# Optimization experiments

Measured on AMD Instinct MI355X. Metric: run time of the kernel, lower is better.

The kernel has to match this reference:

```python
import jax, jax.numpy as jnp
import numpy as np

N_NODES = 100000


def _sage_conv(x, src, dst, Wl, Wr, b):
    # PyG SAGEConv (aggr='mean'): out = lin_l(mean_j x_j) + lin_r(x_i)
    deg = jax.ops.segment_sum(jnp.ones_like(src, dtype=x.dtype), dst, num_segments=N_NODES)
    agg = jax.ops.segment_sum(x[src], dst, num_segments=N_NODES)
    agg = agg / jnp.clip(deg, 1.0)[:, None]
    return agg @ Wl.T + x @ Wr.T + b


def setup_inputs() -> dict:
    key = jax.random.key(0)
    ks = jax.random.split(key, 16)
    N, E, ES = N_NODES, 1600000, 100000
    IN, H, D = 64, 128, 64

    def lin(k, out_c, in_c):
        s = 1.0 / np.sqrt(in_c)
        return jax.random.uniform(k, (out_c, in_c), jnp.float32, -s, s)

    inp = {
        "x": jax.random.normal(ks[0], (N, IN), jnp.float32),
        "edge_index": jax.random.randint(ks[1], (2, E), 0, N, jnp.int64),
        "edge_sample": jax.random.randint(ks[2], (2, ES), 0, N, jnp.int64),
        # SAGEConv 0: 64 -> 128
        "Wl0": lin(ks[3], H, IN), "Wr0": lin(ks[4], H, IN), "b0": jnp.zeros((H,), jnp.float32),
        # SAGEConv 1: 128 -> 128
        "Wl1": lin(ks[5], H, H), "Wr1": lin(ks[6], H, H), "b1": jnp.zeros((H,), jnp.float32),
        # SAGEConv 2: 128 -> 64
        "Wl2": lin(ks[7], D, H), "Wr2": lin(ks[8], D, H), "b2": jnp.zeros((D,), jnp.float32),
        # feature decoder MLP: 64 -> 128 -> 64
        "Wd1": lin(ks[9], H, D), "bd1": jnp.zeros((H,), jnp.float32),
        "Wd2": lin(ks[10], IN, H), "bd2": jnp.zeros((IN,), jnp.float32),
    }
    return inp


def reference(x, edge_index, edge_sample, Wl0, Wr0, b0, Wl1, Wr1, b1, Wl2, Wr2, b2, Wd1, bd1, Wd2, bd2):
    src, dst = edge_index[0], edge_index[1]
    # encoder (dropout = identity at inference)
    h = jax.nn.relu(_sage_conv(x, src, dst, Wl0, Wr0, b0))
    h = jax.nn.relu(_sage_conv(h, src, dst, Wl1, Wr1, b1))
    emb = _sage_conv(h, src, dst, Wl2, Wr2, b2)
    # feature decoder
    rec = jax.nn.relu(emb @ Wd1.T + bd1) @ Wd2.T + bd2
    # edge decoder: dot product
    edge_scores = jnp.sum(emb[edge_sample[0]] * emb[edge_sample[1]], axis=1)
    return emb, rec, edge_scores
```

## Files before the change

### kernel.cpp

```cpp
#include <hip/hip_runtime.h>

#define NN 100000
#define NBK 98
#define CHUNK 8192
typedef unsigned int uint;
typedef unsigned short ushort;

using f32x4 = __attribute__((ext_vector_type(4))) float;
using s16x8 = __attribute__((ext_vector_type(8))) short;

__device__ inline ushort f32_to_bf16(float f) {
  uint u = __float_as_uint(f);
  uint r = (u + 0x7FFFu + ((u >> 16) & 1u)) >> 16;
  return (ushort)r;
}
__device__ inline float bf16_to_f32(ushort h) {
  return __uint_as_float(((uint)h) << 16);
}

typedef __attribute__((address_space(1))) const unsigned int gas_u32;
typedef __attribute__((address_space(3))) unsigned int las_u32;
__device__ __forceinline__ void gld_lds16(const void* gp, void* lp) {
  __builtin_amdgcn_global_load_lds((gas_u32*)gp, (las_u32*)lp, 16, 0, 0);
}

struct P8 { const float* p[8]; };

__global__ void k_prep(const int* __restrict__ dst, uint* __restrict__ bcnt,
                       uint* __restrict__ chunkCnt, int E, int NCB,
                       const float* __restrict__ x, ushort* __restrict__ xb, int n4, int NC,
                       P8 w, ushort* __restrict__ whi, int wtotal) {
  int b = blockIdx.x;
  int tid = threadIdx.x;
  if (b < NCB) {
    __shared__ uint hist[NBK];
    for (int i = tid; i < NBK; i += 256) hist[i] = 0;
    __syncthreads();
    int base = b * CHUNK;
    int lim = min(base + CHUNK, E);
    for (int e = base + tid; e < lim; e += 256) atomicAdd(&hist[(uint)dst[e] >> 10], 1u);
    __syncthreads();
    for (int i = tid; i < NBK; i += 256) {
      uint h = hist[i];
      chunkCnt[(i << 8) + b] = h;
      if (h) atomicAdd(&bcnt[i], h);
    }
  } else if (b < NCB + NC) {
    int i = (b - NCB) * 256 + tid;
    if (i < n4) {
      float4 v = ((const float4*)x)[i];
      uint2 o;
      o.x = (uint)f32_to_bf16(v.x) | ((uint)f32_to_bf16(v.y) << 16);
      o.y = (uint)f32_to_bf16(v.z) | ((uint)f32_to_bf16(v.w) << 16);
      ((uint2*)xb)[i] = o;
    }
  } else {
    int g = (b - NCB - NC) * 256 + tid;
    if (g < wtotal) {
      const int offs[8] = {0, 8192, 16384, 32768, 49152, 57344, 65536, 73728};
      int s = 0;
#pragma unroll
      for (int i = 1; i < 8; ++i) s += (g >= offs[i]);
      whi[g] = f32_to_bf16(w.p[s][g - offs[s]]);
    }
  }
}

__global__ void k_bscan0(const uint* __restrict__ bcnt, uint* __restrict__ bbase,
                         int* __restrict__ rp) {
  if (threadIdx.x == 0) {
    uint s = 0;
    for (int i = 0; i < NBK; ++i) {
      bbase[i] = s;
      s += bcnt[i];
    }
    bbase[NBK] = s;
    rp[NN] = (int)s;
  }
}

__global__ void k_bscan1(const uint* __restrict__ bbase, const uint* __restrict__ chunkCnt,
                         uint* __restrict__ chunkBase, int NCB) {
  int bk = blockIdx.x;
  int l = threadIdx.x;
  uint carry = bbase[bk];
#pragma unroll
  for (int seg = 0; seg < 4; ++seg) {
    int c = seg * 64 + l;
    uint v = (c < NCB) ? chunkCnt[(bk << 8) + c] : 0u;
    uint incl = v;
#pragma unroll
    for (int off = 1; off < 64; off <<= 1) {
      uint t = __shfl_up(incl, off, 64);
      if (l >= off) incl += t;
    }
    if (c < NCB) chunkBase[(bk << 8) + c] = carry + incl - v;
    carry += __shfl(incl, 63, 64);
  }
}

__global__ void k_bscatter(const int* __restrict__ src, const int* __restrict__ dst,
                           const uint* __restrict__ chunkBase, uint* __restrict__ packed, int E) {
  __shared__ uint cur[NBK];
  int tid = threadIdx.x;
  int b = blockIdx.x;
  for (int i = tid; i < NBK; i += 256) cur[i] = chunkBase[(i << 8) + b];
  __syncthreads();
  int base = b * CHUNK;
  int lim = min(base + CHUNK, E);
  for (int e = base + tid; e < lim; e += 256) {
    uint d = (uint)dst[e];
    uint s = (uint)src[e];
    uint bk = d >> 10;
    uint p = atomicAdd(&cur[bk], 1u);
    packed[p] = ((d & 1023u) << 20) | s;
  }
}

__global__ void k_build(const uint* __restrict__ bbase, const uint* __restrict__ packed,
                        int* __restrict__ rp, int* __restrict__ col) {
  __shared__ uint hist[1024];
  __shared__ uint ws[256];
  int b = blockIdx.x;
  int tid = threadIdx.x;
  uint lo = bbase[b], hi = bbase[b + 1];
#pragma unroll
  for (int i = 0; i < 4; ++i) hist[tid + i * 256] = 0;
  __syncthreads();
  for (uint e = lo + tid; e < hi; e += 256) atomicAdd(&hist[packed[e] >> 20], 1u);
  __syncthreads();
  uint v0 = hist[tid * 4], v1 = hist[tid * 4 + 1], v2 = hist[tid * 4 + 2], v3 = hist[tid * 4 + 3];
  ws[tid] = v0 + v1 + v2 + v3;
  __syncthreads();
  for (int off = 1; off < 256; off <<= 1) {
    uint add = (tid >= off) ? ws[tid - off] : 0u;
    __syncthreads();
    ws[tid] += add;
    __syncthreads();
  }
  uint ex = (tid > 0) ? ws[tid - 1] : 0u;
  hist[tid * 4] = ex;
  hist[tid * 4 + 1] = ex + v0;
  hist[tid * 4 + 2] = ex + v0 + v1;
  hist[tid * 4 + 3] = ex + v0 + v1 + v2;
  int nodeBase = b << 10;
#pragma unroll
  for (int i = 0; i < 4; ++i) {
    int node = nodeBase + tid * 4 + i;
    if (node < NN) rp[node] = (int)(lo + hist[tid * 4 + i]);
  }
  __syncthreads();
  for (uint e = lo + tid; e < hi; e += 256) {
    uint pk = packed[e];
    uint p = atomicAdd(&hist[pk >> 20], 1u);
    col[lo + p] = (int)(pk & 0xFFFFFu);
  }
}

#define ACC1(vv) { alo += __uint_as_float((vv) << 16); ahi += __uint_as_float((vv) & 0xffff0000u); }

template <int F, int MODE>
__global__ void k_agg(const ushort* __restrict__ x, const int* __restrict__ rp,
                      const int* __restrict__ col, const float* __restrict__ u,
                      float* __restrict__ of, ushort* __restrict__ ob, int n) {
  constexpr int RS = F / 2;
  int wave = (blockIdx.x * blockDim.x + threadIdx.x) >> 6;
  int lane = threadIdx.x & 63;
  int node, l;
  if (F == 128) { node = wave; l = lane; }
  else { node = wave * 2 + (lane >> 5); l = lane & 31; }
  if (node >= n) return;
  int beg = rp[node], end = rp[node + 1];
  int deg = end - beg;
  const uint* __restrict__ xu = (const uint*)x;
  float alo = 0.f, ahi = 0.f;
  int j = beg;
  for (; j + 8 <= end; j += 8) {
    int c0 = col[j], c1 = col[j + 1], c2 = col[j + 2], c3 = col[j + 3];
    int c4 = col[j + 4], c5 = col[j + 5], c6 = col[j + 6], c7 = col[j + 7];
    uint v0 = xu[(size_t)c0 * RS + l];
    uint v1 = xu[(size_t)c1 * RS + l];
    uint v2 = xu[(size_t)c2 * RS + l];
    uint v3 = xu[(size_t)c3 * RS + l];
    uint v4 = xu[(size_t)c4 * RS + l];
    uint v5 = xu[(size_t)c5 * RS + l];
    uint v6 = xu[(size_t)c6 * RS + l];
    uint v7 = xu[(size_t)c7 * RS + l];
    ACC1(v0) ACC1(v1) ACC1(v2) ACC1(v3) ACC1(v4) ACC1(v5) ACC1(v6) ACC1(v7)
  }
  if (j + 4 <= end) {
    int c0 = col[j], c1 = col[j + 1], c2 = col[j + 2], c3 = col[j + 3];
    uint v0 = xu[(size_t)c0 * RS + l];
    uint v1 = xu[(size_t)c1 * RS + l];
    uint v2 = xu[(size_t)c2 * RS + l];
    uint v3 = xu[(size_t)c3 * RS + l];
    ACC1(v0) ACC1(v1) ACC1(v2) ACC1(v3)
    j += 4;
  }
  for (; j < end; ++j) {
    uint v0 = xu[(size_t)col[j] * RS + l];
    ACC1(v0)
  }
  float inv = 1.0f / (float)(deg > 0 ? deg : 1);
  alo *= inv;
  ahi *= inv;
  if (MODE == 0) {
    ((uint*)ob)[(size_t)node * RS + l] = (uint)f32_to_bf16(alo) | ((uint)f32_to_bf16(ahi) << 16);
  } else {
    float2 uv = ((const float2*)u)[(size_t)node * RS + l];
    float e0 = alo + uv.x, e1 = ahi + uv.y;
    ((float2*)of)[(size_t)node * RS + l] = make_float2(e0, e1);
    ((uint*)ob)[(size_t)node * RS + l] = (uint)f32_to_bf16(e0) | ((uint)f32_to_bf16(e1) << 16);
  }
}

template <int K, int H, bool RELU, bool DUAL, int OUTM>
__global__ __launch_bounds__(256) void k_gemm(
    const ushort* __restrict__ A, const ushort* __restrict__ Wa,
    const ushort* __restrict__ B, const ushort* __restrict__ Wb,
    const float* __restrict__ bias,
    float* __restrict__ outf, ushort* __restrict__ outb, int n) {
  constexpr int BM = 128;
  constexpr int KT = 64;
  constexpr int NKT = K / KT;
  constexpr int MF = (H == 128) ? 4 : 2;
  constexpr int WCH = H / 32;
  __shared__ ushort As[BM * KT];
  __shared__ ushort Ws[H * KT];

  const int tid = threadIdx.x;
  const int lane = tid & 63;
  const int wid = tid >> 6;
  const int fr = lane & 15;
  const int fq = lane >> 4;
  const int blockRow = blockIdx.x * BM;
  const int rowBase = (H == 128) ? (wid >> 1) * 64 : wid * 32;
  const int colBase = (H == 128) ? (wid & 1) * 64 : 0;
  const int srow = lane >> 3;
  const int sslot = (lane & 7) ^ srow;
  const bool fullTile = (blockRow + BM <= n);

  f32x4 acc[MF][4];
#pragma unroll
  for (int mi = 0; mi < MF; ++mi)
#pragma unroll
    for (int ni = 0; ni < 4; ++ni) acc[mi][ni] = (f32x4){0.f, 0.f, 0.f, 0.f};

#pragma unroll
  for (int phase = 0; phase < (DUAL ? 2 : 1); ++phase) {
    const ushort* __restrict__ Ap = phase ? B : A;
    const ushort* __restrict__ Wp = phase ? Wb : Wa;
#pragma unroll
    for (int kt = 0; kt < NKT; ++kt) {
      const int ktb = kt * KT;
      __syncthreads();
      if (fullTile) {
#pragma unroll
        for (int i = 0; i < 4; ++i) {
          int r0 = (wid + i * 4) * 8;
          gld_lds16(Ap + (size_t)(blockRow + r0 + srow) * K + ktb + sslot * 8,
                    (char*)As + r0 * 128);
        }
#pragma unroll
        for (int i = 0; i < WCH; ++i) {
          int r0 = (wid + i * 4) * 8;
          if (WCH >= 4 || wid + i * 4 < WCH * 4)
            gld_lds16(Wp + (size_t)(r0 + srow) * K + ktb + sslot * 8,
                      (char*)Ws + r0 * 128);
        }
      } else {
        for (int c = tid; c < BM * 8; c += 256) {
          int r = c >> 3, kc = c & 7;
          int row = blockRow + r;
          uint4 v = make_uint4(0u, 0u, 0u, 0u);
          if (row < n) v = *(const uint4*)(Ap + (size_t)row * K + ktb + kc * 8);
          *(uint4*)((char*)As + r * 128 + ((kc * 16) ^ ((r & 7) << 4))) = v;
        }
        for (int c = tid; c < H * 8; c += 256) {
          int r = c >> 3, kc = c & 7;
          *(uint4*)((char*)Ws + r * 128 + ((kc * 16) ^ ((r & 7) << 4))) =
              *(const uint4*)(Wp + (size_t)r * K + ktb + kc * 8);
        }
      }
      __syncthreads();
#pragma unroll
      for (int ks = 0; ks < 2; ++ks) {
        const int kb = ks * 64 + fq * 16;
        s16x8 af[MF], wf[4];
#pragma unroll
        for (int mi = 0; mi < MF; ++mi) {
          int r = rowBase + mi * 16 + fr;
          af[mi] = *(const s16x8*)((const char*)As + r * 128 + (kb ^ ((r & 7) << 4)));
        }
#pragma unroll
        for (int ni = 0; ni < 4; ++ni) {
          int r = colBase + ni * 16 + fr;
          wf[ni] = *(const s16x8*)((const char*)Ws + r * 128 + (kb ^ ((r & 7) << 4)));
        }
#pragma unroll
        for (int mi = 0; mi < MF; ++mi)
#pragma unroll
          for (int ni = 0; ni < 4; ++ni)
            acc[mi][ni] = __builtin_amdgcn_mfma_f32_16x16x32_bf16(af[mi], wf[ni], acc[mi][ni], 0, 0, 0);
      }
    }
  }
#pragma unroll
  for (int mi = 0; mi < MF; ++mi) {
#pragma unroll
    for (int ni = 0; ni < 4; ++ni) {
#pragma unroll
      for (int r = 0; r < 4; ++r) {
        int row = blockRow + rowBase + mi * 16 + fq * 4 + r;
        int colI = colBase + ni * 16 + fr;
        if (row < n) {
          float v = acc[mi][ni][r];
          if (OUTM == 3) {
            if (colI < 64)
              outb[(size_t)row * 64 + colI] = f32_to_bf16(v);
            else
              outf[(size_t)row * 64 + (colI - 64)] = v + bias[colI - 64];
          } else {
            if (bias) v += bias[colI];
            if (RELU) v = fmaxf(v, 0.f);
            if (OUTM == 1) outf[(size_t)row * H + colI] = v;
            else outb[(size_t)row * H + colI] = f32_to_bf16(v);
          }
        }
      }
    }
  }
}

__global__ __launch_bounds__(256) void k_dec(
    const ushort* __restrict__ emb, const ushort* __restrict__ Wd1,
    const float* __restrict__ bd1, const ushort* __restrict__ Wd2,
    const float* __restrict__ bd2, float* __restrict__ rec, int n) {
  __shared__ ushort smem[24 * 1024];
  ushort* As = smem;
  ushort* W1 = smem + 8192;
  ushort* W2 = smem + 16384;
  ushort* Hs = smem;

  const int tid = threadIdx.x;
  const int lane = tid & 63;
  const int wid = tid >> 6;
  const int fr = lane & 15;
  const int fq = lane >> 4;
  const int blockRow = blockIdx.x * 128;
  const int rowBase1 = (wid >> 1) * 64;
  const int colBase1 = (wid & 1) * 64;
  const int srow8 = lane >> 3, sl8 = lane & 7;
  const int srow4 = lane >> 4, sl16 = lane & 15;
  const bool fullTile = (blockRow + 128 <= n);

  if (fullTile) {
#pragma unroll
    for (int i = 0; i < 4; ++i) {
      int r0 = (wid + i * 4) * 8;
      gld_lds16(emb + (size_t)(blockRow + r0 + srow8) * 64 + (sl8 ^ srow8) * 8,
                (char*)As + r0 * 128);
    }
#pragma unroll
    for (int i = 0; i < 4; ++i) {
      int r0 = (wid + i * 4) * 8;
      gld_lds16(Wd1 + (size_t)(r0 + srow8) * 64 + (sl8 ^ srow8) * 8, (char*)W1 + r0 * 128);
    }
#pragma unroll
    for (int i = 0; i < 4; ++i) {
      int r0 = (wid + i * 4) * 4;
      int grow = r0 + srow4;
      gld_lds16(Wd2 + (size_t)grow * 128 + (sl16 ^ (grow & 7)) * 8, (char*)W2 + r0 * 256);
    }
  } else {
    for (int c = tid; c < 128 * 8; c += 256) {
      int r = c >> 3, s = c & 7;
      int row = blockRow + r;
      uint4 v = make_uint4(0u, 0u, 0u, 0u);
      if (row < n) v = *(const uint4*)(emb + (size_t)row * 64 + s * 8);
      *(uint4*)((char*)As + r * 128 + ((s ^ (r & 7)) << 4)) = v;
    }
    for (int c = tid; c < 128 * 8; c += 256) {
      int r = c >> 3, s = c & 7;
      *(uint4*)((char*)W1 + r * 128 + ((s ^ (r & 7)) << 4)) =
          *(const uint4*)(Wd1 + (size_t)r * 64 + s * 8);
    }
    for (int c = tid; c < 64 * 16; c += 256) {
      int r = c >> 4, s = c & 15;
      *(uint4*)((char*)W2 + r * 256 + ((s ^ (r & 7)) << 4)) =
          *(const uint4*)(Wd2 + (size_t)r * 128 + s * 8);
    }
  }
  __syncthreads();

  f32x4 a1[4][4];
#pragma unroll
  for (int mi = 0; mi < 4; ++mi)
#pragma unroll
    for (int ni = 0; ni < 4; ++ni) a1[mi][ni] = (f32x4){0.f, 0.f, 0.f, 0.f};
#pragma unroll
  for (int ks = 0; ks < 2; ++ks) {
    s16x8 af[4], wf[4];
#pragma unroll
    for (int mi = 0; mi < 4; ++mi) {
      int r = rowBase1 + mi * 16 + fr;
      af[mi] = *(const s16x8*)((const char*)As + r * 128 + (((ks * 4 + fq) ^ (r & 7)) << 4));
    }
#pragma unroll
    for (int ni = 0; ni < 4; ++ni) {
      int r = colBase1 + ni * 16 + fr;
      wf[ni] = *(const s16x8*)((const char*)W1 + r * 128 + (((ks * 4 + fq) ^ (r & 7)) << 4));
    }
#pragma unroll
    for (int mi = 0; mi < 4; ++mi)
#pragma unroll
      for (int ni = 0; ni < 4; ++ni)
        a1[mi][ni] = __builtin_amdgcn_mfma_f32_16x16x32_bf16(af[mi], wf[ni], a1[mi][ni], 0, 0, 0);
  }
  __syncthreads();
#pragma unroll
  for (int mi = 0; mi < 4; ++mi) {
#pragma unroll
    for (int ni = 0; ni < 4; ++ni) {
#pragma unroll
      for (int r = 0; r < 4; ++r) {
        int rowl = rowBase1 + mi * 16 + fq * 4 + r;
        int colI = colBase1 + ni * 16 + fr;
        float v = fmaxf(a1[mi][ni][r] + bd1[colI], 0.f);
        int byte = rowl * 256 + ((((colI >> 3) ^ (rowl & 7))) << 4) + (colI & 7) * 2;
        *(ushort*)((char*)Hs + byte) = f32_to_bf16(v);
      }
    }
  }
  __syncthreads();

  f32x4 a2[2][4];
#pragma unroll
  for (int mi = 0; mi < 2; ++mi)
#pragma unroll
    for (int ni = 0; ni < 4; ++ni) a2[mi][ni] = (f32x4){0.f, 0.f, 0.f, 0.f};
#pragma unroll
  for (int kk = 0; kk < 4; ++kk) {
    s16x8 af[2], wf[4];
#pragma unroll
    for (int mi = 0; mi < 2; ++mi) {
      int r = wid * 32 + mi * 16 + fr;
      af[mi] = *(const s16x8*)((const char*)Hs + r * 256 + (((kk * 4 + fq) ^ (r & 7)) << 4));
    }
#pragma unroll
    for (int ni = 0; ni < 4; ++ni) {
      int r = ni * 16 + fr;
      wf[ni] = *(const s16x8*)((const char*)W2 + r * 256 + (((kk * 4 + fq) ^ (r & 7)) << 4));
    }
#pragma unroll
    for (int mi = 0; mi < 2; ++mi)
#pragma unroll
      for (int ni = 0; ni < 4; ++ni)
        a2[mi][ni] = __builtin_amdgcn_mfma_f32_16x16x32_bf16(af[mi], wf[ni], a2[mi][ni], 0, 0, 0);
  }
#pragma unroll
  for (int mi = 0; mi < 2; ++mi) {
#pragma unroll
    for (int ni = 0; ni < 4; ++ni) {
#pragma unroll
      for (int r = 0; r < 4; ++r) {
        int row = blockRow + wid * 32 + mi * 16 + fq * 4 + r;
        int colI = ni * 16 + fr;
        if (row < n) rec[(size_t)row * 64 + colI] = a2[mi][ni][r] + bd2[colI];
      }
    }
  }
}

__global__ void k_dot(const float* __restrict__ emb, const int* __restrict__ ea,
                      const int* __restrict__ eb, float* __restrict__ out, int ne) {
  int hw = (blockIdx.x * blockDim.x + threadIdx.x) >> 5;
  int l = threadIdx.x & 31;
  if (hw >= ne) return;
  float2 a = ((const float2*)(emb + (size_t)ea[hw] * 64))[l];
  float2 b = ((const float2*)(emb + (size_t)eb[hw] * 64))[l];
  float v = a.x * b.x + a.y * b.y;
#pragma unroll
  for (int off = 16; off; off >>= 1) v += __shfl_xor(v, off, 64);
  if (l == 0) out[hw] = v;
}

extern "C" void kernel_launch(void* const* d_in, const int* in_sizes, int n_in,
                              void* d_out, int out_size, void* d_ws, size_t ws_size,
                              hipStream_t stream) {
  const float* x = (const float*)d_in[0];
  const int* ei = (const int*)d_in[1];
  const int* es = (const int*)d_in[2];
  const float* b0 = (const float*)d_in[5];
  const float* b1 = (const float*)d_in[8];
  const float* b2 = (const float*)d_in[11];
  const float* bd1 = (const float*)d_in[13];
  const float* bd2 = (const float*)d_in[15];

  const int E = in_sizes[1] / 2;
  const int ES = in_sizes[2] / 2;
  const int* srcv = ei;
  const int* dstv = ei + E;
  const int* ea = es;
  const int* eb = es + ES;

  char* wp = (char*)d_ws;
  auto alloc = [&](size_t bytes) {
    char* p = wp;
    wp += (bytes + 511) & ~(size_t)511;
    return p;
  };
  int* row_ptr = (int*)alloc((NN + 1) * sizeof(int));
  uint* bcnt = (uint*)alloc(NBK * sizeof(uint));
  uint* bbase = (uint*)alloc((NBK + 1) * sizeof(uint));
  uint* chunkCnt = (uint*)alloc((size_t)NBK * 256 * sizeof(uint));
  uint* chunkBase = (uint*)alloc((size_t)NBK * 256 * sizeof(uint));
  uint* packed = (uint*)alloc((size_t)E * sizeof(uint));
  int* colv = (int*)alloc((size_t)E * sizeof(int));
  ushort* xb = (ushort*)alloc((size_t)NN * 64 * 2);
  ushort* aggb = (ushort*)alloc((size_t)NN * 128 * 2);
  ushort* h1b = (ushort*)alloc((size_t)NN * 128 * 2);
  ushort* h2b = (ushort*)alloc((size_t)NN * 128 * 2);
  float* uf = (float*)alloc((size_t)NN * 64 * 4);
  ushort* embb = (ushort*)alloc((size_t)NN * 64 * 2);
  ushort* Whb = (ushort*)alloc(81920 * 2);

  const int WO0 = 0, WO1 = 8192, WO2 = 16384, WO3 = 32768, WO4 = 49152,
            WO6 = 65536, WO7 = 73728;

  float* out_emb = (float*)d_out;
  float* out_rec = out_emb + (size_t)NN * 64;
  float* out_sc = out_rec + (size_t)NN * 64;

  hipMemsetAsync(bcnt, 0, NBK * sizeof(uint), stream);

  P8 wptrs;
  wptrs.p[0] = (const float*)d_in[3];  wptrs.p[1] = (const float*)d_in[4];
  wptrs.p[2] = (const float*)d_in[6];  wptrs.p[3] = (const float*)d_in[7];
  wptrs.p[4] = (const float*)d_in[9];  wptrs.p[5] = (const float*)d_in[10];
  wptrs.p[6] = (const float*)d_in[12]; wptrs.p[7] = (const float*)d_in[14];

  const int NCB = (E + CHUNK - 1) / CHUNK;
  const int n4 = NN * 64 / 4;
  const int NC = (n4 + 255) / 256;
  const int NS = (81920 + 255) / 256;
  k_prep<<<NCB + NC + NS, 256, 0, stream>>>(dstv, bcnt, chunkCnt, E, NCB, x, xb, n4, NC,
                                            wptrs, Whb, 81920);
  k_bscan0<<<1, 64, 0, stream>>>(bcnt, bbase, row_ptr);
  k_bscan1<<<NBK, 64, 0, stream>>>(bbase, chunkCnt, chunkBase, NCB);
  k_bscatter<<<NCB, 256, 0, stream>>>(srcv, dstv, chunkBase, packed, E);
  k_build<<<NBK, 256, 0, stream>>>(bbase, packed, row_ptr, colv);

  const int g64 = (NN + 7) / 8;
  const int g128a = (NN + 3) / 4;
  dim3 gg((NN + 127) / 128);

  k_agg<64, 0><<<g64, 256, 0, stream>>>(xb, row_ptr, colv, nullptr, nullptr, aggb, NN);
  k_gemm<64, 128, true, true, 0><<<gg, 256, 0, stream>>>(
      aggb, Whb + WO0, xb, Whb + WO1, b0, nullptr, h1b, NN);
  k_agg<128, 0><<<g128a, 256, 0, stream>>>(h1b, row_ptr, colv, nullptr, nullptr, aggb, NN);
  k_gemm<128, 128, true, true, 0><<<gg, 256, 0, stream>>>(
      aggb, Whb + WO2, h1b, Whb + WO3, b1, nullptr, h2b, NN);
  k_gemm<128, 128, false, false, 3><<<gg, 256, 0, stream>>>(
      h2b, Whb + WO4, nullptr, nullptr, b2, uf, aggb, NN);
  k_agg<64, 2><<<g64, 256, 0, stream>>>(aggb, row_ptr, colv, uf, out_emb, embb, NN);
  k_dec<<<gg, 256, 0, stream>>>(embb, Whb + WO6, bd1, Whb + WO7, bd2, out_rec, NN);
  k_dot<<<(ES + 7) / 8, 256, 0, stream>>>(out_emb, ea, eb, out_sc, ES);
}
```

Baseline: 340.9 us.

## Double-buffer GEMM K-tiles with async LDS loads and merge bucket scan kernels

The GEMM kernel moves to 32-wide K tiles held in two LDS buffers. The next tile is prefetched with global_load_lds while the current one is computed, using an explicit vmcnt wait and barriers, so global load latency can overlap the MFMA work. The H template parameter is removed and the tile is fixed at 128 output columns. The two bucket-scan kernels are merged into one, with each block computing its own prefix through a wave reduction, which saves a launch and the serial single-thread scan. Smaller K tiles mean more barriers per tile, and the hand-placed waitcnt is fragile.

```diff
diff --git a/kernel.cpp b/kernel.cpp
--- a/kernel.cpp
+++ b/kernel.cpp
@@ -66,24 +66,27 @@
   }
 }
 
-__global__ void k_bscan0(const uint* __restrict__ bcnt, uint* __restrict__ bbase,
-                         int* __restrict__ rp) {
-  if (threadIdx.x == 0) {
-    uint s = 0;
-    for (int i = 0; i < NBK; ++i) {
-      bbase[i] = s;
-      s += bcnt[i];
-    }
-    bbase[NBK] = s;
-    rp[NN] = (int)s;
-  }
-}
-
-__global__ void k_bscan1(const uint* __restrict__ bbase, const uint* __restrict__ chunkCnt,
-                         uint* __restrict__ chunkBase, int NCB) {
+__global__ void k_bscan(const uint* __restrict__ bcnt, uint* __restrict__ bbase,
+                        int* __restrict__ rp, const uint* __restrict__ chunkCnt,
+                        uint* __restrict__ chunkBase, int NCB) {
   int bk = blockIdx.x;
   int l = threadIdx.x;
-  uint carry = bbase[bk];
+  uint p = 0, tot = 0;
+  for (int i = l; i < NBK; i += 64) {
+    uint v = bcnt[i];
+    tot += v;
+    if (i < bk) p += v;
+  }
+#pragma unroll
+  for (int off = 1; off < 64; off <<= 1) {
+    p += __shfl_xor(p, off, 64);
+    tot += __shfl_xor(tot, off, 64);
+  }
+  if (l == 0) {
+    bbase[bk] = p;
+    if (bk == 0) { bbase[NBK] = tot; rp[NN] = (int)tot; }
+  }
+  uint carry = p;
 #pragma unroll
   for (int seg = 0; seg < 4; ++seg) {
     int c = seg * 64 + l;
@@ -214,99 +217,107 @@
   }
 }
 
-template <int K, int H, bool RELU, bool DUAL, int OUTM>
+template <int K, bool RELU, bool DUAL, int OUTM>
 __global__ __launch_bounds__(256) void k_gemm(
     const ushort* __restrict__ A, const ushort* __restrict__ Wa,
     const ushort* __restrict__ B, const ushort* __restrict__ Wb,
     const float* __restrict__ bias,
     float* __restrict__ outf, ushort* __restrict__ outb, int n) {
-  constexpr int BM = 128;
-  constexpr int KT = 64;
-  constexpr int NKT = K / KT;
-  constexpr int MF = (H == 128) ? 4 : 2;
-  constexpr int WCH = H / 32;
-  __shared__ ushort As[BM * KT];
-  __shared__ ushort Ws[H * KT];
+  constexpr int KT = 32;
+  constexpr int TPP = K / KT;
+  constexpr int T = (DUAL ? 2 : 1) * TPP;
+  __shared__ ushort As[2][128 * KT];
+  __shared__ ushort Ws[2][128 * KT];
 
   const int tid = threadIdx.x;
   const int lane = tid & 63;
   const int wid = tid >> 6;
   const int fr = lane & 15;
   const int fq = lane >> 4;
-  const int blockRow = blockIdx.x * BM;
-  const int rowBase = (H == 128) ? (wid >> 1) * 64 : wid * 32;
-  const int colBase = (H == 128) ? (wid & 1) * 64 : 0;
-  const int srow = lane >> 3;
-  const int sslot = (lane & 7) ^ srow;
-  const bool fullTile = (blockRow + BM <= n);
-
-  f32x4 acc[MF][4];
-#pragma unroll
-  for (int mi = 0; mi < MF; ++mi)
+  const int blockRow = blockIdx.x * 128;
+  const int rowBase = (wid >> 1) * 64;
+  const int colBase = (wid & 1) * 64;
+  const int srow = lane >> 2;
+  const int sksrc = (lane & 3) ^ ((lane >> 3) & 3);
+  const bool fullTile = (blockRow + 128 <= n);
+
+  f32x4 acc[4][4];
+#pragma unroll
+  for (int mi = 0; mi < 4; ++mi)
 #pragma unroll
     for (int ni = 0; ni < 4; ++ni) acc[mi][ni] = (f32x4){0.f, 0.f, 0.f, 0.f};
 
-#pragma unroll
-  for (int phase = 0; phase < (DUAL ? 2 : 1); ++phase) {
-    const ushort* __restrict__ Ap = phase ? B : A;
-    const ushort* __restrict__ Wp = phase ? Wb : Wa;
-#pragma unroll
-    for (int kt = 0; kt < NKT; ++kt) {
-      const int ktb = kt * KT;
+  auto stage = [&](int buf, int t) {
+    const ushort* __restrict__ Ap = (DUAL && t >= TPP) ? B : A;
+    const ushort* __restrict__ Wp = (DUAL && t >= TPP) ? Wb : Wa;
+    const int ktb = (t % TPP) * KT;
+#pragma unroll
+    for (int i = 0; i < 2; ++i) {
+      int r0 = (wid + i * 4) * 16;
+      gld_lds16(Ap + (size_t)(blockRow + r0 + srow) * K + ktb + sksrc * 8,
+                (char*)As[buf] + r0 * 64);
+      gld_lds16(Wp + (size_t)(r0 + srow) * K + ktb + sksrc * 8,
+                (char*)Ws[buf] + r0 * 64);
+    }
+  };
+  auto compute = [&](int buf) {
+    s16x8 af[4], wf[4];
+#pragma unroll
+    for (int mi = 0; mi < 4; ++mi) {
+      int r = rowBase + mi * 16 + fr;
+      af[mi] = *(const s16x8*)((const char*)As[buf] + r * 64 + ((fq ^ ((r >> 1) & 3)) << 4));
+    }
+#pragma unroll
+    for (int ni = 0; ni < 4; ++ni) {
+      int r = colBase + ni * 16 + fr;
+      wf[ni] = *(const s16x8*)((const char*)Ws[buf] + r * 64 + ((fq ^ ((r >> 1) & 3)) << 4));
+    }
+#pragma unroll
+    for (int mi = 0; mi < 4; ++mi)
+#pragma unroll
+      for (int ni = 0; ni < 4; ++ni)
+        acc[mi][ni] = __builtin_amdgcn_mfma_f32_16x16x32_bf16(af[mi], wf[ni], acc[mi][ni], 0, 0, 0);
+  };
+
+  if (fullTile) {
+    stage(0, 0);
+#pragma unroll
+    for (int t = 0; t < T; ++t) {
+      if (t + 1 < T) {
+        stage((t + 1) & 1, t + 1);
+        asm volatile("s_waitcnt vmcnt(4)" ::: "memory");
+      } else {
+        asm volatile("s_waitcnt vmcnt(0)" ::: "memory");
+      }
+      __builtin_amdgcn_sched_barrier(0);
+      __builtin_amdgcn_s_barrier();
+      compute(t & 1);
+      if (t + 1 < T) __builtin_amdgcn_s_barrier();
+    }
+  } else {
+#pragma unroll
+    for (int t = 0; t < T; ++t) {
+      const ushort* __restrict__ Ap = (DUAL && t >= TPP) ? B : A;
+      const ushort* __restrict__ Wp = (DUAL && t >= TPP) ? Wb : Wa;
+      const int ktb = (t % TPP) * KT;
       __syncthreads();
-      if (fullTile) {
-#pragma unroll
-        for (int i = 0; i < 4; ++i) {
-          int r0 = (wid + i * 4) * 8;
-          gld_lds16(Ap + (size_t)(blockRow + r0 + srow) * K + ktb + sslot * 8,
-                    (char*)As + r0 * 128);
-        }
-#pragma unroll
-        for (int i = 0; i < WCH; ++i) {
-          int r0 = (wid + i * 4) * 8;
-          if (WCH >= 4 || wid + i * 4 < WCH * 4)
-            gld_lds16(Wp + (size_t)(r0 + srow) * K + ktb + sslot * 8,
-                      (char*)Ws + r0 * 128);
-        }
-      } else {
-        for (int c = tid; c < BM * 8; c += 256) {
-          int r = c >> 3, kc = c & 7;
-          int row = blockRow + r;
-          uint4 v = make_uint4(0u, 0u, 0u, 0u);
-          if (row < n) v = *(const uint4*)(Ap + (size_t)row * K + ktb + kc * 8);
-          *(uint4*)((char*)As + r * 128 + ((kc * 16) ^ ((r & 7) << 4))) = v;
-        }
-        for (int c = tid; c < H * 8; c += 256) {
-          int r = c >> 3, kc = c & 7;
-          *(uint4*)((char*)Ws + r * 128 + ((kc * 16) ^ ((r & 7) << 4))) =
-              *(const uint4*)(Wp + (size_t)r * K + ktb + kc * 8);
-        }
+      for (int c = tid; c < 128 * 4; c += 256) {
+        int r = c >> 2, s = c & 3;
+        int row = blockRow + r;
+        int ds = s ^ ((r >> 1) & 3);
+        uint4 v = make_uint4(0u, 0u, 0u, 0u);
+        if (row < n) v = *(const uint4*)(Ap + (size_t)row * K + ktb + s * 8);
+        *(uint4*)((char*)As[0] + r * 64 + (ds << 4)) = v;
+        *(uint4*)((char*)Ws[0] + r * 64 + (ds << 4)) =
+            *(const uint4*)(Wp + (size_t)r * K + ktb + s * 8);
       }
       __syncthreads();
-#pragma unroll
-      for (int ks = 0; ks < 2; ++ks) {
-        const int kb = ks * 64 + fq * 16;
-        s16x8 af[MF], wf[4];
-#pragma unroll
-        for (int mi = 0; mi < MF; ++mi) {
-          int r = rowBase + mi * 16 + fr;
-          af[mi] = *(const s16x8*)((const char*)As + r * 128 + (kb ^ ((r & 7) << 4)));
-        }
-#pragma unroll
-        for (int ni = 0; ni < 4; ++ni) {
-          int r = colBase + ni * 16 + fr;
-          wf[ni] = *(const s16x8*)((const char*)Ws + r * 128 + (kb ^ ((r & 7) << 4)));
-        }
-#pragma unroll
-        for (int mi = 0; mi < MF; ++mi)
-#pragma unroll
-          for (int ni = 0; ni < 4; ++ni)
-            acc[mi][ni] = __builtin_amdgcn_mfma_f32_16x16x32_bf16(af[mi], wf[ni], acc[mi][ni], 0, 0, 0);
-      }
-    }
-  }
-#pragma unroll
-  for (int mi = 0; mi < MF; ++mi) {
+      compute(0);
+    }
+  }
+
+#pragma unroll
+  for (int mi = 0; mi < 4; ++mi) {
 #pragma unroll
     for (int ni = 0; ni < 4; ++ni) {
 #pragma unroll
@@ -323,8 +334,7 @@
           } else {
             if (bias) v += bias[colI];
             if (RELU) v = fmaxf(v, 0.f);
-            if (OUTM == 1) outf[(size_t)row * H + colI] = v;
-            else outb[(size_t)row * H + colI] = f32_to_bf16(v);
+            outb[(size_t)row * 128 + colI] = f32_to_bf16(v);
           }
         }
       }
@@ -546,8 +556,7 @@
   const int NS = (81920 + 255) / 256;
   k_prep<<<NCB + NC + NS, 256, 0, stream>>>(dstv, bcnt, chunkCnt, E, NCB, x, xb, n4, NC,
                                             wptrs, Whb, 81920);
-  k_bscan0<<<1, 64, 0, stream>>>(bcnt, bbase, row_ptr);
-  k_bscan1<<<NBK, 64, 0, stream>>>(bbase, chunkCnt, chunkBase, NCB);
+  k_bscan<<<NBK, 64, 0, stream>>>(bcnt, bbase, row_ptr, chunkCnt, chunkBase, NCB);
   k_bscatter<<<NCB, 256, 0, stream>>>(srcv, dstv, chunkBase, packed, E);
   k_build<<<NBK, 256, 0, stream>>>(bbase, packed, row_ptr, colv);
 
@@ -556,12 +565,12 @@
   dim3 gg((NN + 127) / 128);
 
   k_agg<64, 0><<<g64, 256, 0, stream>>>(xb, row_ptr, colv, nullptr, nullptr, aggb, NN);
-  k_gemm<64, 128, true, true, 0><<<gg, 256, 0, stream>>>(
+  k_gemm<64, true, true, 0><<<gg, 256, 0, stream>>>(
       aggb, Whb + WO0, xb, Whb + WO1, b0, nullptr, h1b, NN);
   k_agg<128, 0><<<g128a, 256, 0, stream>>>(h1b, row_ptr, colv, nullptr, nullptr, aggb, NN);
-  k_gemm<128, 128, true, true, 0><<<gg, 256, 0, stream>>>(
+  k_gemm<128, true, true, 0><<<gg, 256, 0, stream>>>(
       aggb, Whb + WO2, h1b, Whb + WO3, b1, nullptr, h2b, NN);
-  k_gemm<128, 128, false, false, 3><<<gg, 256, 0, stream>>>(
+  k_gemm<128, false, false, 3><<<gg, 256, 0, stream>>>(
       h2b, Whb + WO4, nullptr, nullptr, b2, uf, aggb, NN);
   k_agg<64, 2><<<g64, 256, 0, stream>>>(aggb, row_ptr, colv, uf, out_emb, embb, NN);
   k_dec<<<gg, 256, 0, stream>>>(embb, Whb + WO6, bd1, Whb + WO7, bd2, out_rec, NN);
```

New measurement: 340.3 us. About the same (-0.2%).
